# Optimization experiments

Hardware: AMD Instinct MI355X
Metric: run time of the kernel (lower is better)

## Reference

```python
import jax, jax.numpy as jnp
import numpy as np

DIM = 1024
HEADS = 16
HEAD_DIM = DIM // HEADS
HIDDEN = int(DIM * 4.0)
EPS = 1e-5


def setup_inputs() -> dict:
    key = jax.random.key(0)
    ks = jax.random.split(key, 16)
    s = 0.02
    inp = {
        'x': jax.random.normal(ks[0], (2, 2048, DIM), dtype=jnp.float32),
        'g1': jnp.ones((DIM,), jnp.float32),
        'b1': jnp.zeros((DIM,), jnp.float32),
        'Wq': jax.random.normal(ks[1], (DIM, DIM)) * s,
        'bq': jnp.zeros((DIM,), jnp.float32),
        'Wk': jax.random.normal(ks[2], (DIM, DIM)) * s,
        'bk': jnp.zeros((DIM,), jnp.float32),
        'Wv': jax.random.normal(ks[3], (DIM, DIM)) * s,
        'bv': jnp.zeros((DIM,), jnp.float32),
        'Wo': jax.random.normal(ks[4], (DIM, DIM)) * s,
        'bo': jnp.zeros((DIM,), jnp.float32),
        'g2': jnp.ones((DIM,), jnp.float32),
        'b2': jnp.zeros((DIM,), jnp.float32),
        'W1': jax.random.normal(ks[5], (DIM, HIDDEN)) * s,
        'bf1': jnp.zeros((HIDDEN,), jnp.float32),
        'W2': jax.random.normal(ks[6], (HIDDEN, DIM)) * s,
        'bf2': jnp.zeros((DIM,), jnp.float32),
    }
    return inp


def _layernorm(x, g, b):
    mu = jnp.mean(x, axis=-1, keepdims=True)
    var = jnp.mean((x - mu) ** 2, axis=-1, keepdims=True)
    return (x - mu) * jax.lax.rsqrt(var + EPS) * g + b


def _block(x, g1, b1, Wq, bq, Wk, bk, Wv, bv, Wo, bo, g2, b2, W1, bf1, W2, bf2):
    B, N, C = x.shape
    h = _layernorm(x, g1, b1)
    # project and split heads: [B, H, N, D]
    q = (h @ Wq + bq).reshape(B, N, HEADS, HEAD_DIM).transpose(0, 2, 1, 3)
    k = (h @ Wk + bk).reshape(B, N, HEADS, HEAD_DIM).transpose(0, 2, 1, 3)
    v = (h @ Wv + bv).reshape(B, N, HEADS, HEAD_DIM).transpose(0, 2, 1, 3)
    scale = HEAD_DIM ** -0.5
    attn = jnp.einsum('bhqd,bhkd->bhqk', q, k) * scale
    attn = jax.nn.softmax(attn, axis=-1)
    o = jnp.einsum('bhqk,bhkd->bhqd', attn, v)
    o = o.transpose(0, 2, 1, 3).reshape(B, N, C)
    x = x + (o @ Wo + bo)
    h = _layernorm(x, g2, b2)
    h = jax.nn.gelu(h @ W1 + bf1, approximate=False)
    x = x + (h @ W2 + bf2)
    return x


def reference(x, g1, b1, Wq, bq, Wk, bk, Wv, bv, Wo, bo, g2, b2, W1, bf1, W2, bf2):
    return _block(x, g1, b1, Wq, bq, Wk, bk, Wv, bv, Wo, bo, g2, b2, W1, bf1, W2, bf2)
```

## Files before the change

kernel.cpp:

```cpp
#include <hip/hip_runtime.h>
#include <hip/hip_bf16.h>
#include <math.h>


typedef unsigned short ushort_t;
typedef short short8 __attribute__((ext_vector_type(8)));
typedef float f32x4 __attribute__((ext_vector_type(4)));

#define TOKENS 4096
#define SEQ    2048
#define DIMC   1024
#define HID    4096

__device__ __forceinline__ float bf2f(ushort_t u) {
    union { float f; unsigned int u; } c; c.u = ((unsigned int)u) << 16; return c.f;
}
__device__ __forceinline__ ushort_t f2bf(float f) {
    union { float f; unsigned int u; } c; c.f = f;
    unsigned int u = c.u;
    unsigned int r = u + 0x7fffu + ((u >> 16) & 1u);
    return (ushort_t)(r >> 16);
}
__device__ __forceinline__ float gelu_f(float x) {
    const float y = 0.79788456080286536f * (x + 0.044715f * x * x * x);
    const float t = __expf(-2.0f * fabsf(y));
    const float th = (1.0f - t) / (1.0f + t);
    return 0.5f * x * (1.0f + copysignf(th, y));
}
__device__ __forceinline__ float load_elem(const void* p, size_t i, int isbf) {
    return isbf ? bf2f(((const ushort_t*)p)[i]) : ((const float*)p)[i];
}

__global__ __launch_bounds__(256) void detect_dtype(
    const ushort_t* __restrict__ x, int* __restrict__ flag)
{
    __shared__ int bad;
    if (threadIdx.x == 0) bad = 0;
    __syncthreads();
    for (int i = threadIdx.x; i < 4096; i += 256) {
        float v = bf2f(x[i]);
        if (!(fabsf(v) <= 1e6f)) bad = 1;
    }
    __syncthreads();
    if (threadIdx.x == 0) { flag[0] = (bad == 0) ? 1 : 0; flag[1] = 1; }
}

__global__ __launch_bounds__(256) void transpose_conv4(
    const void* __restrict__ w0, const void* __restrict__ w1,
    const void* __restrict__ w2, const void* __restrict__ w3,
    ushort_t* __restrict__ outbase, const int* __restrict__ flag)
{
    __shared__ ushort_t tile[32][33];
    const int isbf = *flag;
    const int z = blockIdx.z;
    const void* in = z == 0 ? w0 : (z == 1 ? w1 : (z == 2 ? w2 : w3));
    ushort_t* out = outbase + (size_t)z * DIMC * DIMC;
    const int kb = blockIdx.y * 32, nb = blockIdx.x * 32;
    const int tx = threadIdx.x & 31, ty = threadIdx.x >> 5;
    for (int i = 0; i < 4; i++) {
        int k = kb + ty + i * 8;
        tile[ty + i * 8][tx] = f2bf(load_elem(in, (size_t)k * DIMC + nb + tx, isbf));
    }
    __syncthreads();
    for (int i = 0; i < 4; i++) {
        int n = nb + ty + i * 8;
        out[(size_t)n * DIMC + kb + tx] = tile[tx][ty + i * 8];
    }
}

__global__ __launch_bounds__(256) void transpose_ff(
    const void* __restrict__ W1, const void* __restrict__ W2,
    ushort_t* __restrict__ w1t, ushort_t* __restrict__ w2t,
    const int* __restrict__ flag)
{
    __shared__ ushort_t tile[32][33];
    const int isbf = *flag;
    const int z = blockIdx.z;
    const void* in = z ? W2 : W1;
    ushort_t* out = z ? w2t : w1t;
    const int K = z ? HID : DIMC;
    const int N = z ? DIMC : HID;
    const int bx = z ? blockIdx.y : blockIdx.x;
    const int by = z ? blockIdx.x : blockIdx.y;
    const int kb = by * 32, nb = bx * 32;
    const int tx = threadIdx.x & 31, ty = threadIdx.x >> 5;
    for (int i = 0; i < 4; i++) {
        int k = kb + ty + i * 8;
        tile[ty + i * 8][tx] = f2bf(load_elem(in, (size_t)k * N + nb + tx, isbf));
    }
    __syncthreads();
    for (int i = 0; i < 4; i++) {
        int n = nb + ty + i * 8;
        out[(size_t)n * K + kb + tx] = tile[tx][ty + i * 8];
    }
}

template<int INMODE>
__global__ __launch_bounds__(256) void ln_kernel(
    const void* __restrict__ in, const void* __restrict__ g,
    const void* __restrict__ b, const int* __restrict__ flag,
    ushort_t* __restrict__ out)
{
    const int isbf = *flag;
    const int t = blockIdx.x;
    const int tid = threadIdx.x;
    const size_t base = (size_t)t * DIMC;
    float v[4];
    for (int i = 0; i < 4; i++) {
        int idx = tid + i * 256;
        v[i] = (INMODE == 1) ? ((const float*)in)[base + idx]
                             : load_elem(in, base + idx, isbf);
    }
    float s  = v[0] + v[1] + v[2] + v[3];
    float s2 = v[0]*v[0] + v[1]*v[1] + v[2]*v[2] + v[3]*v[3];
    for (int off = 1; off < 64; off <<= 1) {
        s  += __shfl_xor(s,  off);
        s2 += __shfl_xor(s2, off);
    }
    __shared__ float red[8];
    const int wave = tid >> 6, lane = tid & 63;
    if (lane == 0) { red[wave] = s; red[wave + 4] = s2; }
    __syncthreads();
    s  = red[0] + red[1] + red[2] + red[3];
    s2 = red[4] + red[5] + red[6] + red[7];
    const float mu  = s * (1.0f / DIMC);
    const float var = s2 * (1.0f / DIMC) - mu * mu;
    const float inv = rsqrtf(fmaxf(var, 0.f) + 1e-5f);
    for (int i = 0; i < 4; i++) {
        int idx = tid + i * 256;
        float o = (v[i] - mu) * inv * load_elem(g, idx, isbf) + load_elem(b, idx, isbf);
        out[base + idx] = f2bf(o);
    }
}

template<int BN, int RES, int ACT, int OUTF>
__global__ __launch_bounds__(256) void gemm_bt(
    const ushort_t* __restrict__ A, const ushort_t* __restrict__ BT,
    const void* __restrict__ bias0, const void* __restrict__ bias1,
    const void* __restrict__ bias2, const void* __restrict__ resid,
    void* __restrict__ out0, void* __restrict__ out1, void* __restrict__ out2,
    int M, int N, int K, int Ksub, const int* __restrict__ flag)
{
    constexpr int BM   = 128;
    constexpr int JF   = BN / 32;
    constexpr int ASEG = BM / 16;
    constexpr int SPW  = (BM + BN) / 64;
    __shared__ __align__(16) ushort_t As[BM][32];
    __shared__ __align__(16) ushort_t Bs[BN][32];
    const int isbf = *flag;
    const int tid = threadIdx.x, lane = tid & 63, wave = tid >> 6;
    const int m0 = blockIdx.y * BM, n0 = blockIdx.x * BN;
    const int wm = (wave & 1) * 64;
    const int wn = (wave >> 1) * (BN / 2);
    const int lm = lane & 15, quad = lane >> 4;

    const void* biasp = bias0;
    void* outp = out0;
    int nout = N;
    int colmask = 0x7fffffff;
    int sel = 0;
    if (OUTF == 3) {
        sel = n0 >> 10;
        biasp = sel == 0 ? bias0 : (sel == 1 ? bias1 : bias2);
        outp  = sel == 0 ? out0  : (sel == 1 ? out1  : out2);
        nout = 1024; colmask = 1023;
    }
    int kbeg = 0;
    if (OUTF == 4) {
        kbeg = blockIdx.z * Ksub;
        outp = blockIdx.z ? out1 : out0;
    }

    f32x4 acc[4][JF];
    for (int i = 0; i < 4; i++)
        for (int j = 0; j < JF; j++)
            acc[i][j] = (f32x4){0.f, 0.f, 0.f, 0.f};

    const int lrow = lane >> 2;
    const int lcol = (lane & 3) * 8;

    for (int k0 = kbeg; k0 < kbeg + Ksub; k0 += 32) {
#pragma unroll
        for (int s = 0; s < SPW; s++) {
            const int seg = wave * SPW + s;
            const ushort_t* gp;
            ushort_t* lp;
            if (seg < ASEG) {
                gp = &A[(size_t)(m0 + seg * 16 + lrow) * K + k0 + lcol];
                lp = &As[seg * 16][0];
            } else {
                gp = &BT[(size_t)(n0 + (seg - ASEG) * 16 + lrow) * K + k0 + lcol];
                lp = &Bs[(seg - ASEG) * 16][0];
            }
            __builtin_amdgcn_global_load_lds(
                (const __attribute__((address_space(1))) unsigned int*)gp,
                (__attribute__((address_space(3))) unsigned int*)lp, 16, 0, 0);
        }
        __syncthreads();
        short8 af[4], bfr[JF];
#pragma unroll
        for (int i = 0; i < 4; i++) af[i] = *(const short8*)&As[wm + i * 16 + lm][quad * 8];
#pragma unroll
        for (int j = 0; j < JF; j++) bfr[j] = *(const short8*)&Bs[wn + j * 16 + lm][quad * 8];
#pragma unroll
        for (int i = 0; i < 4; i++)
#pragma unroll
            for (int j = 0; j < JF; j++)
                acc[i][j] = __builtin_amdgcn_mfma_f32_16x16x32_bf16(af[i], bfr[j], acc[i][j], 0, 0, 0);
        __syncthreads();
    }

    if (OUTF == 3 && sel == 2) {
        for (int j = 0; j < JF; j++) {
            const int colo = (n0 + wn + j * 16 + lm) & 1023;
            const float bv = load_elem(biasp, colo, isbf);
            for (int i = 0; i < 4; i++) {
                const int token = m0 + wm + i * 16 + quad * 4;
                const int bb = token >> 11, ss = token & 2047;
                unsigned int lo = (unsigned int)f2bf(acc[i][j][0] + bv)
                                | ((unsigned int)f2bf(acc[i][j][1] + bv) << 16);
                unsigned int hi = (unsigned int)f2bf(acc[i][j][2] + bv)
                                | ((unsigned int)f2bf(acc[i][j][3] + bv) << 16);
                *(uint2*)&((ushort_t*)outp)[(size_t)((bb << 10) + colo) * SEQ + ss] =
                    make_uint2(lo, hi);
            }
        }
        return;
    }

    for (int j = 0; j < JF; j++) {
        const int col  = n0 + wn + j * 16 + lm;
        const int colo = col & colmask;
        const float bv = (OUTF == 4) ? 0.f : load_elem(biasp, colo, isbf);
        for (int i = 0; i < 4; i++) {
            const int rbase = m0 + wm + i * 16 + quad * 4;
            for (int r = 0; r < 4; r++) {
                const size_t oi = (size_t)(rbase + r) * nout + colo;
                float v2 = acc[i][j][r] + bv;
                if (ACT == 1) v2 = gelu_f(v2);
                if (RES == 1) v2 += load_elem(resid, oi, isbf);
                if (RES == 2) v2 += ((const float*)resid)[oi];
                if (OUTF == 1 || OUTF == 4) { ((float*)outp)[oi] = v2; }
                else if (OUTF == 2) {
                    if (isbf) ((ushort_t*)outp)[oi] = f2bf(v2);
                    else      ((float*)outp)[oi] = v2;
                }
                else                { ((ushort_t*)outp)[oi] = f2bf(v2); }
            }
        }
    }
}

__global__ __launch_bounds__(256) void splitk_reduce(
    const float* __restrict__ p0, const float* __restrict__ p1,
    const void* __restrict__ bias, const float* __restrict__ resid,
    void* __restrict__ out, const int* __restrict__ flag)
{
    const int isbf = *flag;
    const size_t i = ((size_t)blockIdx.x * 256 + threadIdx.x) * 4;
    const float4 a = *(const float4*)&p0[i];
    const float4 b = *(const float4*)&p1[i];
    const float4 r = *(const float4*)&resid[i];
    const int col = (int)(i & 1023);
    float v[4];
    v[0] = a.x + b.x + r.x + load_elem(bias, col + 0, isbf);
    v[1] = a.y + b.y + r.y + load_elem(bias, col + 1, isbf);
    v[2] = a.z + b.z + r.z + load_elem(bias, col + 2, isbf);
    v[3] = a.w + b.w + r.w + load_elem(bias, col + 3, isbf);
    if (isbf) {
        unsigned int lo = (unsigned int)f2bf(v[0]) | ((unsigned int)f2bf(v[1]) << 16);
        unsigned int hi = (unsigned int)f2bf(v[2]) | ((unsigned int)f2bf(v[3]) << 16);
        *(uint2*)&((ushort_t*)out)[i] = make_uint2(lo, hi);
    } else {
        *(float4*)&((float*)out)[i] = make_float4(v[0], v[1], v[2], v[3]);
    }
}

__global__ __launch_bounds__(256) void attn_kernel(
    const ushort_t* __restrict__ q, const ushort_t* __restrict__ k,
    const ushort_t* __restrict__ vt, ushort_t* __restrict__ o)
{
    const int bh = blockIdx.x;
    const int b  = bh >> 4, h = bh & 15;
    const int q0 = blockIdx.y * 128;
    const int tid = threadIdx.x, lane = tid & 63, wave = tid >> 6;
    const int lm = lane & 15, quad = lane >> 4;

    __shared__ ushort_t Qs[128][72];
    __shared__ ushort_t Ks[64][72];
    __shared__ ushort_t Vt[64][72];
    __shared__ ushort_t Ps[4][32][72];

    const size_t base  = ((size_t)b * SEQ) * DIMC + h * 64;
    const size_t vbase = ((size_t)b * DIMC + h * 64) * SEQ;

    {
        const int er0 = (tid * 8) >> 6;
        const int ec0 = (tid * 8) & 63;
        for (int half = 0; half < 4; half++) {
            const int r = er0 + half * 32;
            short8 qq = *(const short8*)&q[base + (size_t)(q0 + r) * DIMC + ec0];
            short8 qs;
            for (int i = 0; i < 8; i++)
                qs[i] = (short)f2bf(bf2f((ushort_t)qq[i]) * 0.18033688011112042f);
            *(short8*)&Qs[r][ec0] = qs;
        }
    }
    __syncthreads();

    short8 qf[2][2];
    for (int qh = 0; qh < 2; qh++)
        for (int ks = 0; ks < 2; ks++)
            qf[qh][ks] = *(const short8*)&Qs[wave * 32 + qh * 16 + lm][quad * 8 + ks * 32];

    short8 onef;
    for (int i = 0; i < 8; i++) onef[i] = (short)0x3F80;

    f32x4 oacc[4][2], lacc[2];
    for (int j = 0; j < 4; j++)
        for (int qh = 0; qh < 2; qh++) oacc[j][qh] = (f32x4){0.f, 0.f, 0.f, 0.f};
    lacc[0] = (f32x4){0.f, 0.f, 0.f, 0.f};
    lacc[1] = (f32x4){0.f, 0.f, 0.f, 0.f};

    const int er = (tid * 8) >> 6;
    const int ec = (tid * 8) & 63;
    const int dd = tid >> 2;
    const int kg = tid & 3;

    short8 kreg0, kreg1, vreg0, vreg1;
    {
        kreg0 = *(const short8*)&k[base + (size_t)(er) * DIMC + ec];
        kreg1 = *(const short8*)&k[base + (size_t)(er + 32) * DIMC + ec];
        const size_t vsrc = vbase + (size_t)dd * SEQ + kg * 16;
        vreg0 = *(const short8*)&vt[vsrc];
        vreg1 = *(const short8*)&vt[vsrc + 8];
    }

    for (int kt = 0; kt < SEQ / 64; kt++) {
        __syncthreads();
        *(short8*)&Ks[er][ec]          = kreg0;
        *(short8*)&Ks[er + 32][ec]     = kreg1;
        *(short8*)&Vt[dd][kg * 16]     = vreg0;
        *(short8*)&Vt[dd][kg * 16 + 8] = vreg1;
        __syncthreads();
        if (kt + 1 < SEQ / 64) {
            const int kn = (kt + 1) * 64;
            kreg0 = *(const short8*)&k[base + (size_t)(kn + er) * DIMC + ec];
            kreg1 = *(const short8*)&k[base + (size_t)(kn + er + 32) * DIMC + ec];
            const size_t vsrc = vbase + (size_t)dd * SEQ + kn + kg * 16;
            vreg0 = *(const short8*)&vt[vsrc];
            vreg1 = *(const short8*)&vt[vsrc + 8];
        }

        f32x4 st[4][2];
        for (int j = 0; j < 4; j++)
            for (int qh = 0; qh < 2; qh++) st[j][qh] = (f32x4){0.f, 0.f, 0.f, 0.f};
        for (int ks = 0; ks < 2; ks++) {
            for (int j = 0; j < 4; j++) {
                short8 kf = *(const short8*)&Ks[j * 16 + lm][quad * 8 + ks * 32];
                for (int qh = 0; qh < 2; qh++)
                    st[j][qh] = __builtin_amdgcn_mfma_f32_16x16x32_bf16(kf, qf[qh][ks], st[j][qh], 0, 0, 0);
            }
        }

        for (int j = 0; j < 4; j++)
            for (int qh = 0; qh < 2; qh++) {
                unsigned int u0 = __float_as_uint(__builtin_amdgcn_exp2f(st[j][qh][0]));
                unsigned int u1 = __float_as_uint(__builtin_amdgcn_exp2f(st[j][qh][1]));
                unsigned int u2 = __float_as_uint(__builtin_amdgcn_exp2f(st[j][qh][2]));
                unsigned int u3 = __float_as_uint(__builtin_amdgcn_exp2f(st[j][qh][3]));
                unsigned int lo = (u1 & 0xffff0000u) | (u0 >> 16);
                unsigned int hi = (u3 & 0xffff0000u) | (u2 >> 16);
                *(uint2*)&Ps[wave][qh * 16 + lm][j * 16 + quad * 4] = make_uint2(lo, hi);
            }

        for (int ks = 0; ks < 2; ks++) {
            for (int qh = 0; qh < 2; qh++) {
                short8 pf = *(const short8*)&Ps[wave][qh * 16 + lm][quad * 8 + ks * 32];
                lacc[qh] = __builtin_amdgcn_mfma_f32_16x16x32_bf16(pf, onef, lacc[qh], 0, 0, 0);
                for (int j = 0; j < 4; j++) {
                    short8 vf = *(const short8*)&Vt[j * 16 + lm][quad * 8 + ks * 32];
                    oacc[j][qh] = __builtin_amdgcn_mfma_f32_16x16x32_bf16(pf, vf, oacc[j][qh], 0, 0, 0);
                }
            }
        }
    }

    float rinv[2][4];
    for (int qh = 0; qh < 2; qh++)
        for (int r = 0; r < 4; r++) rinv[qh][r] = 1.0f / fmaxf(lacc[qh][r], 1e-30f);

    for (int j = 0; j < 4; j++)
        for (int qh = 0; qh < 2; qh++)
            for (int r = 0; r < 4; r++) {
                const int row = q0 + wave * 32 + qh * 16 + quad * 4 + r;
                o[base + (size_t)row * DIMC + j * 16 + lm] = f2bf(oacc[j][qh][r] * rinv[qh][r]);
            }
}

extern "C" void kernel_launch(void* const* d_in, const int* in_sizes, int n_in,
                              void* d_out, int out_size, void* d_ws, size_t ws_size,
                              hipStream_t stream)
{
    const void* x   = d_in[0];
    const void* g1  = d_in[1];
    const void* b1  = d_in[2];
    const void* Wq  = d_in[3];
    const void* bq  = d_in[4];
    const void* Wk  = d_in[5];
    const void* bk  = d_in[6];
    const void* Wv  = d_in[7];
    const void* bv  = d_in[8];
    const void* Wo  = d_in[9];
    const void* bo  = d_in[10];
    const void* g2  = d_in[11];
    const void* b2  = d_in[12];
    const void* W1  = d_in[13];
    const void* bf1 = d_in[14];
    const void* W2  = d_in[15];
    const void* bf2 = d_in[16];

    const size_t SZ_TOKD_BF = (size_t)TOKENS * DIMC * 2;
    const size_t SZ_TOKD_F  = (size_t)TOKENS * DIMC * 4;
    const size_t SZ_W_SQ    = (size_t)DIMC * DIMC * 2;
    const size_t SZ_W_FF    = (size_t)DIMC * HID * 2;
    const size_t SZ_FF1     = (size_t)TOKENS * HID * 2;

    char* ws = (char*)d_ws;
    size_t off = 0;
    int*      flag = (int*)(ws + off);       off += 256;
    ushort_t* h    = (ushort_t*)(ws + off);  off += SZ_TOKD_BF;
    ushort_t* qb   = (ushort_t*)(ws + off);  off += SZ_TOKD_BF;
    ushort_t* kb_  = (ushort_t*)(ws + off);  off += SZ_TOKD_BF;
    ushort_t* ao   = (ushort_t*)(ws + off);  off += SZ_TOKD_BF;
    ushort_t* vtg  = (ushort_t*)(ws + off);  off += SZ_TOKD_BF;
    float*    x1f  = (float*)qb;
    float*    p0   = (float*)ao;
    ushort_t* wqt  = (ushort_t*)(ws + off);  off += SZ_W_SQ;
    ushort_t* wkt  = (ushort_t*)(ws + off);  off += SZ_W_SQ;
    ushort_t* wvt  = (ushort_t*)(ws + off);  off += SZ_W_SQ;
    ushort_t* wot  = (ushort_t*)(ws + off);  off += SZ_W_SQ;
    ushort_t* w1t  = (ushort_t*)(ws + off);  off += SZ_W_FF;
    ushort_t* w2t  = (ushort_t*)(ws + off);  off += SZ_W_FF;
    ushort_t* ff1  = (ushort_t*)(ws + off);  off += SZ_FF1;
    float*    p1   = (float*)(ws + off);     off += SZ_TOKD_F;
    if (ws_size < off) return;

    (void)wkt; (void)wvt;

    detect_dtype<<<1, 256, 0, stream>>>((const ushort_t*)x, flag);

    transpose_conv4<<<dim3(32, 32, 4), 256, 0, stream>>>(Wq, Wk, Wv, Wo, wqt, flag);
    transpose_ff<<<dim3(128, 32, 2), 256, 0, stream>>>(W1, W2, w1t, w2t, flag);

    ln_kernel<0><<<TOKENS, 256, 0, stream>>>(x, g1, b1, flag, h);

    gemm_bt<128, 0, 0, 3><<<dim3(24, 32), 256, 0, stream>>>(
        h, wqt, bq, bk, bv, nullptr, qb, kb_, vtg, TOKENS, 3072, DIMC, DIMC, flag);

    attn_kernel<<<dim3(32, 16), 256, 0, stream>>>(qb, kb_, vtg, ao);

    gemm_bt<64, 1, 0, 1><<<dim3(16, 32), 256, 0, stream>>>(
        ao, wot, bo, nullptr, nullptr, x, x1f, nullptr, nullptr, TOKENS, DIMC, DIMC, DIMC, flag);

    ln_kernel<1><<<TOKENS, 256, 0, stream>>>(x1f, g2, b2, flag, h);

    gemm_bt<128, 0, 1, 0><<<dim3(32, 32), 256, 0, stream>>>(
        h, w1t, bf1, nullptr, nullptr, nullptr, ff1, nullptr, nullptr, TOKENS, HID, DIMC, DIMC, flag);

    gemm_bt<64, 0, 0, 4><<<dim3(16, 32, 2), 256, 0, stream>>>(
        ff1, w2t, nullptr, nullptr, nullptr, nullptr, p0, p1, nullptr,
        TOKENS, DIMC, HID, HID / 2, flag);

    splitk_reduce<<<TOKENS * DIMC / 1024, 256, 0, stream>>>(p0, p1, bf2, x1f, d_out, flag);
}
```

Before: 442.4 us.

## Merge weight transposes, shrink GEMM tiles, split-K the output projection

Fuses the two weight-transpose launches into a single flat-grid kernel. Switches the QKV and FF1 GEMMs from 128-wide to 64-wide N tiles, doubling their grid sizes. Runs the Wo projection as a two-way split-K GEMM followed by a templated reduce that adds bias and the raw input residual. The goal is better CU occupancy on these GEMMs and fewer launches, at the cost of extra fp32 partial traffic and one additional reduce kernel.

```diff
diff --git a/kernel.cpp b/kernel.cpp
--- a/kernel.cpp
+++ b/kernel.cpp
@@ -45,43 +45,31 @@
     if (threadIdx.x == 0) { flag[0] = (bad == 0) ? 1 : 0; flag[1] = 1; }
 }
 
-__global__ __launch_bounds__(256) void transpose_conv4(
-    const void* __restrict__ w0, const void* __restrict__ w1,
-    const void* __restrict__ w2, const void* __restrict__ w3,
-    ushort_t* __restrict__ outbase, const int* __restrict__ flag)
+__global__ __launch_bounds__(256) void transpose_w_all(
+    const void* __restrict__ Wq, const void* __restrict__ Wk,
+    const void* __restrict__ Wv, const void* __restrict__ Wo,
+    const void* __restrict__ W1, const void* __restrict__ W2,
+    ushort_t* __restrict__ wsq, ushort_t* __restrict__ w1t,
+    ushort_t* __restrict__ w2t, const int* __restrict__ flag)
 {
     __shared__ ushort_t tile[32][33];
     const int isbf = *flag;
-    const int z = blockIdx.z;
-    const void* in = z == 0 ? w0 : (z == 1 ? w1 : (z == 2 ? w2 : w3));
-    ushort_t* out = outbase + (size_t)z * DIMC * DIMC;
-    const int kb = blockIdx.y * 32, nb = blockIdx.x * 32;
-    const int tx = threadIdx.x & 31, ty = threadIdx.x >> 5;
-    for (int i = 0; i < 4; i++) {
-        int k = kb + ty + i * 8;
-        tile[ty + i * 8][tx] = f2bf(load_elem(in, (size_t)k * DIMC + nb + tx, isbf));
-    }
-    __syncthreads();
-    for (int i = 0; i < 4; i++) {
-        int n = nb + ty + i * 8;
-        out[(size_t)n * DIMC + kb + tx] = tile[tx][ty + i * 8];
-    }
-}
-
-__global__ __launch_bounds__(256) void transpose_ff(
-    const void* __restrict__ W1, const void* __restrict__ W2,
-    ushort_t* __restrict__ w1t, ushort_t* __restrict__ w2t,
-    const int* __restrict__ flag)
-{
-    __shared__ ushort_t tile[32][33];
-    const int isbf = *flag;
-    const int z = blockIdx.z;
-    const void* in = z ? W2 : W1;
-    ushort_t* out = z ? w2t : w1t;
-    const int K = z ? HID : DIMC;
-    const int N = z ? DIMC : HID;
-    const int bx = z ? blockIdx.y : blockIdx.x;
-    const int by = z ? blockIdx.x : blockIdx.y;
+    const int id = blockIdx.x;
+    const void* in; ushort_t* out; int K, N, bx, by;
+    if (id < 4096) {
+        const int z = id >> 10, t = id & 1023;
+        in = z == 0 ? Wq : (z == 1 ? Wk : (z == 2 ? Wv : Wo));
+        out = wsq + (size_t)z * DIMC * DIMC;
+        K = DIMC; N = DIMC; bx = t & 31; by = t >> 5;
+    } else if (id < 8192) {
+        const int t = id - 4096;
+        in = W1; out = w1t; K = DIMC; N = HID;
+        bx = t & 127; by = t >> 7;
+    } else {
+        const int t = id - 8192;
+        in = W2; out = w2t; K = HID; N = DIMC;
+        bx = t & 31; by = t >> 5;
+    }
     const int kb = by * 32, nb = bx * 32;
     const int tx = threadIdx.x & 31, ty = threadIdx.x >> 5;
     for (int i = 0; i < 4; i++) {
@@ -251,23 +239,25 @@
     }
 }
 
+template<int RESRAW, int OUTF32>
 __global__ __launch_bounds__(256) void splitk_reduce(
     const float* __restrict__ p0, const float* __restrict__ p1,
-    const void* __restrict__ bias, const float* __restrict__ resid,
+    const void* __restrict__ bias, const void* __restrict__ resid,
     void* __restrict__ out, const int* __restrict__ flag)
 {
     const int isbf = *flag;
     const size_t i = ((size_t)blockIdx.x * 256 + threadIdx.x) * 4;
     const float4 a = *(const float4*)&p0[i];
     const float4 b = *(const float4*)&p1[i];
-    const float4 r = *(const float4*)&resid[i];
     const int col = (int)(i & 1023);
-    float v[4];
-    v[0] = a.x + b.x + r.x + load_elem(bias, col + 0, isbf);
-    v[1] = a.y + b.y + r.y + load_elem(bias, col + 1, isbf);
-    v[2] = a.z + b.z + r.z + load_elem(bias, col + 2, isbf);
-    v[3] = a.w + b.w + r.w + load_elem(bias, col + 3, isbf);
-    if (isbf) {
+    float v[4] = {a.x + b.x, a.y + b.y, a.z + b.z, a.w + b.w};
+    for (int c = 0; c < 4; c++) {
+        v[c] += load_elem(bias, col + c, isbf);
+        v[c] += RESRAW ? load_elem(resid, i + c, isbf) : ((const float*)resid)[i + c];
+    }
+    if (OUTF32) {
+        *(float4*)&((float*)out)[i] = make_float4(v[0], v[1], v[2], v[3]);
+    } else if (isbf) {
         unsigned int lo = (unsigned int)f2bf(v[0]) | ((unsigned int)f2bf(v[1]) << 16);
         unsigned int hi = (unsigned int)f2bf(v[2]) | ((unsigned int)f2bf(v[3]) << 16);
         *(uint2*)&((ushort_t*)out)[i] = make_uint2(lo, hi);
@@ -435,6 +425,7 @@
     ushort_t* ao   = (ushort_t*)(ws + off);  off += SZ_TOKD_BF;
     ushort_t* vtg  = (ushort_t*)(ws + off);  off += SZ_TOKD_BF;
     float*    x1f  = (float*)qb;
+    float*    pa   = (float*)qb;
     float*    p0   = (float*)ao;
     ushort_t* wqt  = (ushort_t*)(ws + off);  off += SZ_W_SQ;
     ushort_t* wkt  = (ushort_t*)(ws + off);  off += SZ_W_SQ;
@@ -450,27 +441,33 @@
 
     detect_dtype<<<1, 256, 0, stream>>>((const ushort_t*)x, flag);
 
-    transpose_conv4<<<dim3(32, 32, 4), 256, 0, stream>>>(Wq, Wk, Wv, Wo, wqt, flag);
-    transpose_ff<<<dim3(128, 32, 2), 256, 0, stream>>>(W1, W2, w1t, w2t, flag);
+    transpose_w_all<<<12288, 256, 0, stream>>>(Wq, Wk, Wv, Wo, W1, W2,
+                                               wqt, w1t, w2t, flag);
 
     ln_kernel<0><<<TOKENS, 256, 0, stream>>>(x, g1, b1, flag, h);
 
-    gemm_bt<128, 0, 0, 3><<<dim3(24, 32), 256, 0, stream>>>(
+    gemm_bt<64, 0, 0, 3><<<dim3(48, 32), 256, 0, stream>>>(
         h, wqt, bq, bk, bv, nullptr, qb, kb_, vtg, TOKENS, 3072, DIMC, DIMC, flag);
 
     attn_kernel<<<dim3(32, 16), 256, 0, stream>>>(qb, kb_, vtg, ao);
 
-    gemm_bt<64, 1, 0, 1><<<dim3(16, 32), 256, 0, stream>>>(
-        ao, wot, bo, nullptr, nullptr, x, x1f, nullptr, nullptr, TOKENS, DIMC, DIMC, DIMC, flag);
+    gemm_bt<64, 0, 0, 4><<<dim3(16, 32, 2), 256, 0, stream>>>(
+        ao, wot, nullptr, nullptr, nullptr, nullptr, pa, p1, nullptr,
+        TOKENS, DIMC, DIMC, DIMC / 2, flag);
+
+    splitk_reduce<1, 1><<<TOKENS * DIMC / 1024, 256, 0, stream>>>(
+        pa, p1, bo, x, x1f, flag);
 
     ln_kernel<1><<<TOKENS, 256, 0, stream>>>(x1f, g2, b2, flag, h);
 
-    gemm_bt<128, 0, 1, 0><<<dim3(32, 32), 256, 0, stream>>>(
-        h, w1t, bf1, nullptr, nullptr, nullptr, ff1, nullptr, nullptr, TOKENS, HID, DIMC, DIMC, flag);
+    gemm_bt<64, 0, 1, 0><<<dim3(64, 32), 256, 0, stream>>>(
+        h, w1t, bf1, nullptr, nullptr, nullptr, ff1, nullptr, nullptr,
+        TOKENS, HID, DIMC, DIMC, flag);
 
     gemm_bt<64, 0, 0, 4><<<dim3(16, 32, 2), 256, 0, stream>>>(
         ff1, w2t, nullptr, nullptr, nullptr, nullptr, p0, p1, nullptr,
         TOKENS, DIMC, HID, HID / 2, flag);
 
-    splitk_reduce<<<TOKENS * DIMC / 1024, 256, 0, stream>>>(p0, p1, bf2, x1f, d_out, flag);
-}
+    splitk_reduce<0, 0><<<TOKENS * DIMC / 1024, 256, 0, stream>>>(
+        p0, p1, bf2, x1f, d_out, flag);
+}
```

New measurement: 417.7 us. -5.6%, faster.
